# Kernel optimization log

Measured on AMD Instinct MI355X. Metric: run time of the kernel, lower is better.

Reference implementation:

```python
import jax, jax.numpy as jnp
import numpy as np

QMAX = 127.0  # int8 symmetric
EPS = 1e-8


def _fake_quant(v, scale):
    # quantize/clamp/dequantize with straight-through rounding (STE clip)
    s = jnp.maximum(scale, EPS)
    scaled = v / s
    clipped = jnp.clip(scaled, -QMAX, QMAX)
    q = clipped + jax.lax.stop_gradient(jnp.round(clipped) - clipped)
    return q * s


def setup_inputs() -> dict:
    key = jax.random.key(0)
    kx, kw, kb = jax.random.split(key, 3)
    B, S, D_IN, D_OUT = 8, 2048, 4096, 4096
    x = jax.random.normal(kx, (B, S, D_IN), dtype=jnp.float32)
    weight = jax.random.normal(kw, (D_OUT, D_IN), dtype=jnp.float32) * 0.02
    bias = jax.random.normal(kb, (D_OUT,), dtype=jnp.float32) * 0.02
    return {"x": x, "weight": weight, "bias": bias}


def reference(x, weight, bias):
    # activation: dynamic per-tensor symmetric int8 fake-quant
    a_scale = jnp.max(jnp.abs(x)) / QMAX
    xq = _fake_quant(x, a_scale)
    # weight: per-channel (output-channel axis 0) symmetric int8 fake-quant
    w_scale = jnp.max(jnp.abs(weight), axis=1, keepdims=True) / QMAX  # [out, 1]
    wq = _fake_quant(weight, w_scale)
    # F.linear: y = x @ W^T + b
    return jnp.einsum('bsd,od->bso', xq, wq) + bias
```

## Files before the change

### kernel.cpp

```cpp
#include <hip/hip_runtime.h>
#include <hip/hip_bf16.h>
#include <stdint.h>


#define QMAX_F 127.0f
#define EPS_F 1e-8f

typedef int v4i __attribute__((ext_vector_type(4)));

static constexpr size_t WSCALE_OFF = 64;
static constexpr size_t XQ_OFF = 1u << 16;

__global__ void absmax_kernel(const float4* __restrict__ x, unsigned* __restrict__ out, int n4) {
    int tid = blockIdx.x * blockDim.x + threadIdx.x;
    int stride = gridDim.x * blockDim.x;
    float m = 0.0f;
    for (int i = tid; i < n4; i += stride) {
        float4 v = x[i];
        m = fmaxf(m, fmaxf(fmaxf(fabsf(v.x), fabsf(v.y)), fmaxf(fabsf(v.z), fabsf(v.w))));
    }
    for (int off = 32; off > 0; off >>= 1)
        m = fmaxf(m, __shfl_xor(m, off));
    __shared__ float wmax[4];
    int lane = threadIdx.x & 63, wid = threadIdx.x >> 6;
    if (lane == 0) wmax[wid] = m;
    __syncthreads();
    if (threadIdx.x == 0) {
        float b = fmaxf(fmaxf(wmax[0], wmax[1]), fmaxf(wmax[2], wmax[3]));
        atomicMax(out, __float_as_uint(b));
    }
}

__device__ __forceinline__ int quant1(float v, float s) {
    float t = v / s;
    t = fminf(fmaxf(t, -QMAX_F), QMAX_F);
    return (int)rintf(t);
}

__global__ void quantx_kernel(const float4* __restrict__ x, const unsigned* __restrict__ amax,
                              int* __restrict__ xq, int n4) {
    float s = fmaxf(__uint_as_float(*amax) / QMAX_F, EPS_F);
    int tid = blockIdx.x * blockDim.x + threadIdx.x;
    int stride = gridDim.x * blockDim.x;
    for (int i = tid; i < n4; i += stride) {
        float4 v = x[i];
        int q0 = quant1(v.x, s), q1 = quant1(v.y, s), q2 = quant1(v.z, s), q3 = quant1(v.w, s);
        xq[i] = (q0 & 0xff) | ((q1 & 0xff) << 8) | ((q2 & 0xff) << 16) | ((q3 & 0xff) << 24);
    }
}

__global__ void quantw_kernel(const float4* __restrict__ w, int* __restrict__ wq,
                              float* __restrict__ w_scale, int K4) {
    int row = blockIdx.x;
    const float4* wr = w + (size_t)row * K4;
    int t = threadIdx.x;
    float4 vals[4];
    float m = 0.0f;
    for (int i = 0; i < 4; i++) {
        float4 v = wr[t + 256 * i];
        vals[i] = v;
        m = fmaxf(m, fmaxf(fmaxf(fabsf(v.x), fabsf(v.y)), fmaxf(fabsf(v.z), fabsf(v.w))));
    }
    for (int off = 32; off > 0; off >>= 1)
        m = fmaxf(m, __shfl_xor(m, off));
    __shared__ float sm[4];
    if ((t & 63) == 0) sm[t >> 6] = m;
    __syncthreads();
    float mb = fmaxf(fmaxf(sm[0], sm[1]), fmaxf(sm[2], sm[3]));
    float s = fmaxf(mb / QMAX_F, EPS_F);
    if (t == 0) w_scale[row] = s;
    int* wqr = wq + (size_t)row * K4;
    for (int i = 0; i < 4; i++) {
        float4 v = vals[i];
        int q0 = quant1(v.x, s), q1 = quant1(v.y, s), q2 = quant1(v.z, s), q3 = quant1(v.w, s);
        wqr[t + 256 * i] = (q0 & 0xff) | ((q1 & 0xff) << 8) | ((q2 & 0xff) << 16) | ((q3 & 0xff) << 24);
    }
}

#define BM 256
#define BN 256
#define BKB 128

__device__ __forceinline__ void gload16(const char* g, char* l) {
    __builtin_amdgcn_global_load_lds(
        (const __attribute__((address_space(1))) void*)g,
        (__attribute__((address_space(3))) void*)l, 16, 0, 0);
}

__global__ __launch_bounds__(512, 2) void gemm_i8_8ph(
    const char* __restrict__ xq, const char* __restrict__ wq,
    const float* __restrict__ w_scale, const unsigned* __restrict__ amax,
    const float* __restrict__ bias, float* __restrict__ out,
    int M, int N, int K) {
    __shared__ __align__(16) char lds[131072];

    const int nwg = gridDim.x, bid = blockIdx.x;
    const int cpx = nwg >> 3;
    const int swz = (bid & 7) * cpx + (bid >> 3);
    const int nbm = M / BM;
    const int bm = swz % nbm, bn = swz / nbm;

    const int t = threadIdx.x;
    const int lane = t & 63, wid = t >> 6;
    const int wr = wid >> 2, wc = wid & 3;

    const int srow = t >> 3;
    const int scol = ((t & 7) ^ (srow & 7)) << 4;
    const char* aSrc = xq + (size_t)(bm * BM + srow) * K + scol;
    const char* bSrc = wq + (size_t)(bn * BN + srow) * K + scol;
    char* ldsT = lds + t * 16;

    auto stageA = [&](int half, int tt, int ktc) {
        char* d = ldsT + ((unsigned)(tt & 1) << 16) + ((unsigned)half << 14);
        gload16(aSrc + (size_t)(half * 128) * K + ktc, d);
        gload16(aSrc + (size_t)(half * 128 + 64) * K + ktc, d + 8192);
    };
    auto stageB = [&](int half, int tt, int ktc) {
        char* d = ldsT + ((unsigned)(tt & 1) << 16) + 32768u + ((unsigned)half << 14);
        gload16(bSrc + (size_t)(half * 128) * K + ktc, d);
        gload16(bSrc + (size_t)(half * 128 + 64) * K + ktc, d + 8192);
    };

    const int rA = lane & 15, kg = lane >> 4, sw7 = lane & 7;
    const unsigned cks0 = (unsigned)((kg ^ sw7) << 4);
    const unsigned cks1 = (unsigned)(((4 + kg) ^ sw7) << 4);
    const unsigned aBase = ((unsigned)wr << 14) + ((unsigned)rA << 7);
    const unsigned bBase = 32768u + ((unsigned)wc << 13) + ((unsigned)rA << 7);

    v4i acc[8][4];
#pragma unroll
    for (int m = 0; m < 8; m++)
#pragma unroll
        for (int n = 0; n < 4; n++) acc[m][n] = (v4i){0, 0, 0, 0};

    const int nkt = K / BKB;

    stageA(0, 0, 0); stageA(1, 0, 0); stageB(0, 0, 0); stageB(1, 0, 0);
    {
        const int k1 = (1 < nkt) ? BKB : 0;
        stageB(0, 1, k1); stageA(0, 1, k1); stageB(1, 1, k1);
    }
    asm volatile("s_waitcnt vmcnt(6)" ::: "memory");
    __builtin_amdgcn_s_barrier();

    for (int T = 0; T < nkt; ++T) {
        const unsigned bb = (unsigned)(T & 1) << 16;
        const int kA1 = (T + 1 < nkt) ? (T + 1) * BKB : 0;
        const int kT2 = (T + 2 < nkt) ? (T + 2) * BKB : 0;
        v4i a[4][2], b0[2][2], b1[2][2];

#pragma unroll
        for (int m = 0; m < 4; m++) {
            a[m][0] = *(const v4i*)(lds + bb + aBase + ((unsigned)m << 11) + cks0);
            a[m][1] = *(const v4i*)(lds + bb + aBase + ((unsigned)m << 11) + cks1);
        }
#pragma unroll
        for (int n = 0; n < 2; n++) {
            b0[n][0] = *(const v4i*)(lds + bb + bBase + ((unsigned)n << 11) + cks0);
            b0[n][1] = *(const v4i*)(lds + bb + bBase + ((unsigned)n << 11) + cks1);
        }
        stageA(1, T + 1, kA1);
        __builtin_amdgcn_s_barrier();
        asm volatile("s_waitcnt lgkmcnt(0)" ::: "memory");
        __builtin_amdgcn_sched_barrier(0);
        __builtin_amdgcn_s_setprio(1);
#pragma unroll
        for (int ks = 0; ks < 2; ks++)
#pragma unroll
            for (int m = 0; m < 4; m++)
#pragma unroll
                for (int n = 0; n < 2; n++)
                    acc[m][n] = __builtin_amdgcn_mfma_i32_16x16x64_i8(a[m][ks], b0[n][ks], acc[m][n], 0, 0, 0);
        __builtin_amdgcn_s_setprio(0);

#pragma unroll
        for (int n = 0; n < 2; n++) {
            b1[n][0] = *(const v4i*)(lds + bb + bBase + 4096u + ((unsigned)n << 11) + cks0);
            b1[n][1] = *(const v4i*)(lds + bb + bBase + 4096u + ((unsigned)n << 11) + cks1);
        }
        __builtin_amdgcn_s_barrier();
        asm volatile("s_waitcnt lgkmcnt(0)" ::: "memory");
        __builtin_amdgcn_sched_barrier(0);
        __builtin_amdgcn_s_setprio(1);
#pragma unroll
        for (int ks = 0; ks < 2; ks++)
#pragma unroll
            for (int m = 0; m < 4; m++)
#pragma unroll
                for (int n = 0; n < 2; n++)
                    acc[m][2 + n] = __builtin_amdgcn_mfma_i32_16x16x64_i8(a[m][ks], b1[n][ks], acc[m][2 + n], 0, 0, 0);
        __builtin_amdgcn_s_setprio(0);

#pragma unroll
        for (int m = 0; m < 4; m++) {
            a[m][0] = *(const v4i*)(lds + bb + aBase + 8192u + ((unsigned)m << 11) + cks0);
            a[m][1] = *(const v4i*)(lds + bb + aBase + 8192u + ((unsigned)m << 11) + cks1);
        }
        __builtin_amdgcn_s_barrier();
        asm volatile("s_waitcnt lgkmcnt(0)" ::: "memory");
        __builtin_amdgcn_sched_barrier(0);
        __builtin_amdgcn_s_setprio(1);
#pragma unroll
        for (int ks = 0; ks < 2; ks++)
#pragma unroll
            for (int m = 0; m < 4; m++)
#pragma unroll
                for (int n = 0; n < 2; n++)
                    acc[4 + m][2 + n] = __builtin_amdgcn_mfma_i32_16x16x64_i8(a[m][ks], b1[n][ks], acc[4 + m][2 + n], 0, 0, 0);
        __builtin_amdgcn_s_setprio(0);

        stageB(0, T + 2, kT2);
        stageA(0, T + 2, kT2);
        stageB(1, T + 2, kT2);
        asm volatile("s_waitcnt vmcnt(6)" ::: "memory");
        __builtin_amdgcn_s_barrier();
        __builtin_amdgcn_s_setprio(1);
#pragma unroll
        for (int ks = 0; ks < 2; ks++)
#pragma unroll
            for (int m = 0; m < 4; m++)
#pragma unroll
                for (int n = 0; n < 2; n++)
                    acc[4 + m][n] = __builtin_amdgcn_mfma_i32_16x16x64_i8(a[m][ks], b0[n][ks], acc[4 + m][n], 0, 0, 0);
        __builtin_amdgcn_s_setprio(0);
    }

    float a_s = fmaxf(__uint_as_float(*amax) / QMAX_F, EPS_F);
    const int row0 = bm * BM + wr * 128;
    const int col0 = bn * BN + wc * 64;
#pragma unroll
    for (int n = 0; n < 4; n++) {
        int col = col0 + n * 16 + rA;
        float f = a_s * w_scale[col];
        float bv = bias[col];
#pragma unroll
        for (int m = 0; m < 8; m++) {
            int row = row0 + m * 16 + (kg << 2);
            size_t base = (size_t)row * N + col;
#pragma unroll
            for (int j = 0; j < 4; j++)
                out[base + (size_t)j * N] = (float)acc[m][n][j] * f + bv;
        }
    }
}

extern "C" void kernel_launch(void* const* d_in, const int* in_sizes, int n_in,
                              void* d_out, int out_size, void* d_ws, size_t ws_size,
                              hipStream_t stream) {
    const float* x = (const float*)d_in[0];
    const float* w = (const float*)d_in[1];
    const float* bias = (const float*)d_in[2];
    float* out = (float*)d_out;

    const int N = in_sizes[2];
    const int K = in_sizes[1] / N;
    const int M = in_sizes[0] / K;

    char* ws = (char*)d_ws;
    unsigned* amax = (unsigned*)ws;
    float* w_scale = (float*)(ws + WSCALE_OFF);
    char* xq = ws + XQ_OFF;
    char* wq = ws + XQ_OFF + (size_t)M * K;

    size_t needed = XQ_OFF + (size_t)M * K + (size_t)N * K;
    if (ws_size < needed) return;

    hipMemsetAsync(amax, 0, 4, stream);

    int n4x = (M * K) / 4;
    absmax_kernel<<<2048, 256, 0, stream>>>((const float4*)x, amax, n4x);
    quantx_kernel<<<2048, 256, 0, stream>>>((const float4*)x, amax, (int*)xq, n4x);
    quantw_kernel<<<N, 256, 0, stream>>>((const float4*)w, (int*)wq, w_scale, K / 4);

    int grid = (M / BM) * (N / BN);
    gemm_i8_8ph<<<grid, 512, 0, stream>>>(xq, wq, w_scale, amax, bias, out, M, N, K);
}
```

Before: 444.7 us.

## Fuse absmax and weight quant into one prep kernel, split LDS waits in GEMM

Merges the activation absmax reduction and the per-row weight quantization into a single kernel launched with one block per output row, which removes a launch. Quantization now multiplies by a reciprocal scale instead of dividing, which can change rounding at .5 boundaries. In the GEMM main loop the A-fragment LDS reads are split into two halves with a partial lgkmcnt wait, so the first half of the MFMAs can start while the rest of the reads are still in flight. This risks extra scheduling constraints from the added sched_barriers.

```diff
diff --git a/kernel.cpp b/kernel.cpp
--- a/kernel.cpp
+++ b/kernel.cpp
@@ -11,69 +11,66 @@
 static constexpr size_t WSCALE_OFF = 64;
 static constexpr size_t XQ_OFF = 1u << 16;
 
-__global__ void absmax_kernel(const float4* __restrict__ x, unsigned* __restrict__ out, int n4) {
-    int tid = blockIdx.x * blockDim.x + threadIdx.x;
-    int stride = gridDim.x * blockDim.x;
-    float m = 0.0f;
-    for (int i = tid; i < n4; i += stride) {
-        float4 v = x[i];
-        m = fmaxf(m, fmaxf(fmaxf(fabsf(v.x), fabsf(v.y)), fmaxf(fabsf(v.z), fabsf(v.w))));
-    }
-    for (int off = 32; off > 0; off >>= 1)
-        m = fmaxf(m, __shfl_xor(m, off));
-    __shared__ float wmax[4];
-    int lane = threadIdx.x & 63, wid = threadIdx.x >> 6;
-    if (lane == 0) wmax[wid] = m;
-    __syncthreads();
-    if (threadIdx.x == 0) {
-        float b = fmaxf(fmaxf(wmax[0], wmax[1]), fmaxf(wmax[2], wmax[3]));
-        atomicMax(out, __float_as_uint(b));
-    }
-}
-
-__device__ __forceinline__ int quant1(float v, float s) {
-    float t = v / s;
+__device__ __forceinline__ int quant1m(float v, float rs) {
+    float t = v * rs;
     t = fminf(fmaxf(t, -QMAX_F), QMAX_F);
     return (int)rintf(t);
+}
+
+__global__ void prep_kernel(const float4* __restrict__ x, int nx4,
+                            const float4* __restrict__ w, int* __restrict__ wq,
+                            float* __restrict__ w_scale, int K4,
+                            unsigned* __restrict__ amax) {
+    const int t = threadIdx.x;
+    const int row = blockIdx.x;
+
+    float xm = 0.0f;
+    for (int i = blockIdx.x * 256 + t; i < nx4; i += gridDim.x * 256) {
+        float4 v = x[i];
+        xm = fmaxf(xm, fmaxf(fmaxf(fabsf(v.x), fabsf(v.y)), fmaxf(fabsf(v.z), fabsf(v.w))));
+    }
+
+    const float4* wr = w + (size_t)row * K4;
+    float4 vals[4];
+    float wm = 0.0f;
+    for (int i = 0; i < 4; i++) {
+        float4 v = wr[t + 256 * i];
+        vals[i] = v;
+        wm = fmaxf(wm, fmaxf(fmaxf(fabsf(v.x), fabsf(v.y)), fmaxf(fabsf(v.z), fabsf(v.w))));
+    }
+
+    for (int off = 32; off > 0; off >>= 1) {
+        xm = fmaxf(xm, __shfl_xor(xm, off));
+        wm = fmaxf(wm, __shfl_xor(wm, off));
+    }
+    __shared__ float sx[4], sw[4];
+    if ((t & 63) == 0) { sx[t >> 6] = xm; sw[t >> 6] = wm; }
+    __syncthreads();
+    float xb = fmaxf(fmaxf(sx[0], sx[1]), fmaxf(sx[2], sx[3]));
+    float wb = fmaxf(fmaxf(sw[0], sw[1]), fmaxf(sw[2], sw[3]));
+    if (t == 0) atomicMax(amax, __float_as_uint(xb));
+
+    float s = fmaxf(wb / QMAX_F, EPS_F);
+    if (t == 0) w_scale[row] = s;
+    float rs = 1.0f / s;
+    int* wqr = wq + (size_t)row * K4;
+    for (int i = 0; i < 4; i++) {
+        float4 v = vals[i];
+        int q0 = quant1m(v.x, rs), q1 = quant1m(v.y, rs), q2 = quant1m(v.z, rs), q3 = quant1m(v.w, rs);
+        wqr[t + 256 * i] = (q0 & 0xff) | ((q1 & 0xff) << 8) | ((q2 & 0xff) << 16) | ((q3 & 0xff) << 24);
+    }
 }
 
 __global__ void quantx_kernel(const float4* __restrict__ x, const unsigned* __restrict__ amax,
                               int* __restrict__ xq, int n4) {
     float s = fmaxf(__uint_as_float(*amax) / QMAX_F, EPS_F);
+    float rs = 1.0f / s;
     int tid = blockIdx.x * blockDim.x + threadIdx.x;
     int stride = gridDim.x * blockDim.x;
     for (int i = tid; i < n4; i += stride) {
         float4 v = x[i];
-        int q0 = quant1(v.x, s), q1 = quant1(v.y, s), q2 = quant1(v.z, s), q3 = quant1(v.w, s);
+        int q0 = quant1m(v.x, rs), q1 = quant1m(v.y, rs), q2 = quant1m(v.z, rs), q3 = quant1m(v.w, rs);
         xq[i] = (q0 & 0xff) | ((q1 & 0xff) << 8) | ((q2 & 0xff) << 16) | ((q3 & 0xff) << 24);
-    }
-}
-
-__global__ void quantw_kernel(const float4* __restrict__ w, int* __restrict__ wq,
-                              float* __restrict__ w_scale, int K4) {
-    int row = blockIdx.x;
-    const float4* wr = w + (size_t)row * K4;
-    int t = threadIdx.x;
-    float4 vals[4];
-    float m = 0.0f;
-    for (int i = 0; i < 4; i++) {
-        float4 v = wr[t + 256 * i];
-        vals[i] = v;
-        m = fmaxf(m, fmaxf(fmaxf(fabsf(v.x), fabsf(v.y)), fmaxf(fabsf(v.z), fabsf(v.w))));
-    }
-    for (int off = 32; off > 0; off >>= 1)
-        m = fmaxf(m, __shfl_xor(m, off));
-    __shared__ float sm[4];
-    if ((t & 63) == 0) sm[t >> 6] = m;
-    __syncthreads();
-    float mb = fmaxf(fmaxf(sm[0], sm[1]), fmaxf(sm[2], sm[3]));
-    float s = fmaxf(mb / QMAX_F, EPS_F);
-    if (t == 0) w_scale[row] = s;
-    int* wqr = wq + (size_t)row * K4;
-    for (int i = 0; i < 4; i++) {
-        float4 v = vals[i];
-        int q0 = quant1(v.x, s), q1 = quant1(v.y, s), q2 = quant1(v.z, s), q3 = quant1(v.w, s);
-        wqr[t + 256 * i] = (q0 & 0xff) | ((q1 & 0xff) << 8) | ((q2 & 0xff) << 16) | ((q3 & 0xff) << 24);
     }
 }
 
@@ -150,24 +147,39 @@
         v4i a[4][2], b0[2][2], b1[2][2];
 
 #pragma unroll
-        for (int m = 0; m < 4; m++) {
-            a[m][0] = *(const v4i*)(lds + bb + aBase + ((unsigned)m << 11) + cks0);
-            a[m][1] = *(const v4i*)(lds + bb + aBase + ((unsigned)m << 11) + cks1);
-        }
-#pragma unroll
         for (int n = 0; n < 2; n++) {
             b0[n][0] = *(const v4i*)(lds + bb + bBase + ((unsigned)n << 11) + cks0);
             b0[n][1] = *(const v4i*)(lds + bb + bBase + ((unsigned)n << 11) + cks1);
         }
+#pragma unroll
+        for (int m = 0; m < 2; m++) {
+            a[m][0] = *(const v4i*)(lds + bb + aBase + ((unsigned)m << 11) + cks0);
+            a[m][1] = *(const v4i*)(lds + bb + aBase + ((unsigned)m << 11) + cks1);
+        }
+        __builtin_amdgcn_sched_barrier(0);
+#pragma unroll
+        for (int m = 2; m < 4; m++) {
+            a[m][0] = *(const v4i*)(lds + bb + aBase + ((unsigned)m << 11) + cks0);
+            a[m][1] = *(const v4i*)(lds + bb + aBase + ((unsigned)m << 11) + cks1);
+        }
         stageA(1, T + 1, kA1);
         __builtin_amdgcn_s_barrier();
+        asm volatile("s_waitcnt lgkmcnt(4)" ::: "memory");
+        __builtin_amdgcn_sched_barrier(0);
+        __builtin_amdgcn_s_setprio(1);
+#pragma unroll
+        for (int ks = 0; ks < 2; ks++)
+#pragma unroll
+            for (int m = 0; m < 2; m++)
+#pragma unroll
+                for (int n = 0; n < 2; n++)
+                    acc[m][n] = __builtin_amdgcn_mfma_i32_16x16x64_i8(a[m][ks], b0[n][ks], acc[m][n], 0, 0, 0);
         asm volatile("s_waitcnt lgkmcnt(0)" ::: "memory");
         __builtin_amdgcn_sched_barrier(0);
-        __builtin_amdgcn_s_setprio(1);
-#pragma unroll
-        for (int ks = 0; ks < 2; ks++)
-#pragma unroll
-            for (int m = 0; m < 4; m++)
+#pragma unroll
+        for (int ks = 0; ks < 2; ks++)
+#pragma unroll
+            for (int m = 2; m < 4; m++)
 #pragma unroll
                 for (int n = 0; n < 2; n++)
                     acc[m][n] = __builtin_amdgcn_mfma_i32_16x16x64_i8(a[m][ks], b0[n][ks], acc[m][n], 0, 0, 0);
@@ -192,18 +204,33 @@
         __builtin_amdgcn_s_setprio(0);
 
 #pragma unroll
-        for (int m = 0; m < 4; m++) {
+        for (int m = 0; m < 2; m++) {
             a[m][0] = *(const v4i*)(lds + bb + aBase + 8192u + ((unsigned)m << 11) + cks0);
             a[m][1] = *(const v4i*)(lds + bb + aBase + 8192u + ((unsigned)m << 11) + cks1);
         }
+        __builtin_amdgcn_sched_barrier(0);
+#pragma unroll
+        for (int m = 2; m < 4; m++) {
+            a[m][0] = *(const v4i*)(lds + bb + aBase + 8192u + ((unsigned)m << 11) + cks0);
+            a[m][1] = *(const v4i*)(lds + bb + aBase + 8192u + ((unsigned)m << 11) + cks1);
+        }
         __builtin_amdgcn_s_barrier();
+        asm volatile("s_waitcnt lgkmcnt(4)" ::: "memory");
+        __builtin_amdgcn_sched_barrier(0);
+        __builtin_amdgcn_s_setprio(1);
+#pragma unroll
+        for (int ks = 0; ks < 2; ks++)
+#pragma unroll
+            for (int m = 0; m < 2; m++)
+#pragma unroll
+                for (int n = 0; n < 2; n++)
+                    acc[4 + m][2 + n] = __builtin_amdgcn_mfma_i32_16x16x64_i8(a[m][ks], b1[n][ks], acc[4 + m][2 + n], 0, 0, 0);
         asm volatile("s_waitcnt lgkmcnt(0)" ::: "memory");
         __builtin_amdgcn_sched_barrier(0);
-        __builtin_amdgcn_s_setprio(1);
-#pragma unroll
-        for (int ks = 0; ks < 2; ks++)
-#pragma unroll
-            for (int m = 0; m < 4; m++)
+#pragma unroll
+        for (int ks = 0; ks < 2; ks++)
+#pragma unroll
+            for (int m = 2; m < 4; m++)
 #pragma unroll
                 for (int n = 0; n < 2; n++)
                     acc[4 + m][2 + n] = __builtin_amdgcn_mfma_i32_16x16x64_i8(a[m][ks], b1[n][ks], acc[4 + m][2 + n], 0, 0, 0);
@@ -268,9 +295,9 @@
     hipMemsetAsync(amax, 0, 4, stream);
 
     int n4x = (M * K) / 4;
-    absmax_kernel<<<2048, 256, 0, stream>>>((const float4*)x, amax, n4x);
+    prep_kernel<<<N, 256, 0, stream>>>((const float4*)x, n4x, (const float4*)w,
+                                       (int*)wq, w_scale, K / 4, amax);
     quantx_kernel<<<2048, 256, 0, stream>>>((const float4*)x, amax, (int*)xq, n4x);
-    quantw_kernel<<<N, 256, 0, stream>>>((const float4*)w, (int*)wq, w_scale, K / 4);
 
     int grid = (M / BM) * (N / BN);
     gemm_i8_8ph<<<grid, 512, 0, stream>>>(xq, wq, w_scale, amax, bias, out, M, N, K);
```

Measured after the change: 437.0 us. Within noise of the previous version (-1.7%).
